# Kernel tuning notes

Hardware: AMD Instinct MI355X
Metric: run time of the kernel (lower is better)

## Reference

```python
import jax, jax.numpy as jnp
import numpy as np

LN_EPS = 1e-5  # torch LayerNorm default
MODES = 4


def setup_inputs() -> dict:
    key = jax.random.key(0)
    ks = jax.random.split(key, 5)
    B, S, H = 4, 4096, 1024
    nh, dk = 16, H // 16
    scale = 1.0 / (H * H)
    # frequency mode selection: random shuffle of range(S//2), take 4, sorted (seeded for determinism)
    rng = np.random.default_rng(0)
    index = jnp.asarray(np.sort(rng.permutation(S // 2)[:MODES]).astype(np.int32))
    return {
        "x": jax.random.normal(ks[0], (B, S, H), dtype=jnp.float32),
        "Wq": jax.random.normal(ks[1], (H, H), dtype=jnp.float32) * np.sqrt(2.0 / (H + dk)),
        "bq": jnp.zeros((H,), dtype=jnp.float32),
        "wr": scale * jax.random.uniform(ks[2], (nh, dk, dk, MODES), dtype=jnp.float32),
        "wi": scale * jax.random.uniform(ks[3], (nh, dk, dk, MODES), dtype=jnp.float32),
        "gamma": jnp.ones((H,), dtype=jnp.float32),
        "beta": jnp.zeros((H,), dtype=jnp.float32),
        "index": index,
    }


def reference(x, Wq, bq, wr, wi, gamma, beta, index):
    B, S, H = x.shape
    nh, dk = wr.shape[0], wr.shape[1]
    # q projection and head split: (B,S,H) -> (B,S,nh,dk) -> (B,nh,dk,S)
    q = (x @ Wq.T + bq).reshape(B, S, nh, dk).transpose(0, 2, 3, 1)
    x_ft = jnp.fft.rfft(q, axis=-1)                 # (B,nh,dk,S//2+1) complex
    xm = x_ft[..., index]                           # gather selected modes: (B,nh,dk,M)
    w = wr + 1j * wi                                # (nh,dk,dk,M) complex
    ym = jnp.einsum('bhim,hiom->bhom', xm, w)       # per-mode complex matmul
    # faithful: results written at slots 0..M-1 of out_ft (loop writes out_ft[...,wi])
    out_ft = jnp.zeros((B, nh, dk, S // 2 + 1), dtype=ym.dtype).at[..., :ym.shape[-1]].set(ym)
    x_if = jnp.fft.irfft(out_ft, n=S, axis=-1)      # (B,nh,dk,S) real
    # faithful permute(0,3,2,1).view: flattens as dk-major over heads
    out = x_if.transpose(0, 3, 2, 1).reshape(B, S, H)
    # dropout is identity in eval mode
    y = out + x
    mu = jnp.mean(y, axis=-1, keepdims=True)
    var = jnp.var(y, axis=-1, keepdims=True)
    return (y - mu) * jax.lax.rsqrt(var + LN_EPS) * gamma + beta
```

## Files before the change

### kernel.cpp

```cpp
#include <hip/hip_runtime.h>
#include <math.h>

#define BB 4
#define SS 4096
#define HH 1024
#define NH 16
#define DK 64
#define NMODES 4
#define NSB 32
#define SCHUNK (SS/NSB)
#define NJB (HH/256)
#define TWO_PI 6.28318530717958647692f

__global__ __launch_bounds__(256) void kA_dft(const float* __restrict__ x,
                                              const int* __restrict__ index,
                                              float* __restrict__ P) {
    __shared__ float tab[SCHUNK * 8];
    int t = threadIdx.x;
    int bid = blockIdx.x;
    int sb = bid & (NSB - 1);
    int jb = (bid >> 5) & (NJB - 1);
    int b  = bid >> 7;

    int kk0 = index[0], kk1 = index[1], kk2 = index[2], kk3 = index[3];
    for (int u = t; u < SCHUNK * NMODES; u += 256) {
        int sl = u >> 2, m = u & 3;
        int k = (m == 0) ? kk0 : (m == 1) ? kk1 : (m == 2) ? kk2 : kk3;
        int sv = sb * SCHUNK + sl;
        int r = (k * sv) & (SS - 1);
        float ang = (float)r * (TWO_PI / (float)SS);
        float sn, cs;
        sincosf(ang, &sn, &cs);
        tab[sl * 8 + m * 2]     = cs;
        tab[sl * 8 + m * 2 + 1] = sn;
    }
    __syncthreads();

    int j = jb * 256 + t;
    float acc[8] = {0.f,0.f,0.f,0.f,0.f,0.f,0.f,0.f};
    const float* xp = x + ((size_t)(b * SS + sb * SCHUNK)) * HH + j;
    for (int r = 0; r < SCHUNK; ++r) {
        float xv = xp[(size_t)r * HH];
        float4 t0 = *(const float4*)&tab[r * 8];
        float4 t1 = *(const float4*)&tab[r * 8 + 4];
        acc[0] += xv * t0.x;  acc[1] -= xv * t0.y;
        acc[2] += xv * t0.z;  acc[3] -= xv * t0.w;
        acc[4] += xv * t1.x;  acc[5] -= xv * t1.y;
        acc[6] += xv * t1.z;  acc[7] -= xv * t1.w;
    }
    float* pp = P + ((size_t)((b * NSB + sb) * HH + j)) * 8;
    *(float4*)pp       = make_float4(acc[0], acc[1], acc[2], acc[3]);
    *(float4*)(pp + 4) = make_float4(acc[4], acc[5], acc[6], acc[7]);
}

__global__ __launch_bounds__(256) void kA2_reduce(const float* __restrict__ P,
                                                  float* __restrict__ G) {
    int g = blockIdx.x * 256 + threadIdx.x;
    int q = g & 7;
    int j = (g >> 3) & (HH - 1);
    int b = g >> 13;
    float s = 0.f;
    for (int sb = 0; sb < NSB; ++sb)
        s += P[((size_t)((b * NSB + sb) * HH + j)) * 8 + q];
    G[g] = s;
}

__global__ __launch_bounds__(256) void kB_proj(const float* __restrict__ Wq,
                                               const float* __restrict__ bq,
                                               const int* __restrict__ index,
                                               const float* __restrict__ G,
                                               float* __restrict__ XM) {
    __shared__ float Gs[HH * 8];
    int t = threadIdx.x;
    int cb = blockIdx.x & 15;
    int b  = blockIdx.x >> 4;
    for (int u = t; u < HH * 8; u += 256) Gs[u] = G[(size_t)b * HH * 8 + u];
    __syncthreads();

    int cl = t >> 2, jq = t & 3;
    int c = cb * 64 + cl;
    float acc[8] = {0.f,0.f,0.f,0.f,0.f,0.f,0.f,0.f};
    for (int j0 = jq * 4; j0 < HH; j0 += 16) {
        float4 wv = *(const float4*)&Wq[(size_t)c * HH + j0];
        const float* gp = &Gs[j0 * 8];
        #pragma unroll
        for (int q = 0; q < 8; ++q) acc[q] += wv.x * gp[q];
        #pragma unroll
        for (int q = 0; q < 8; ++q) acc[q] += wv.y * gp[8 + q];
        #pragma unroll
        for (int q = 0; q < 8; ++q) acc[q] += wv.z * gp[16 + q];
        #pragma unroll
        for (int q = 0; q < 8; ++q) acc[q] += wv.w * gp[24 + q];
    }
    #pragma unroll
    for (int q = 0; q < 8; ++q) {
        acc[q] += __shfl_xor(acc[q], 1);
        acc[q] += __shfl_xor(acc[q], 2);
    }
    if (jq == 0) {
        float bias = bq[c];
        #pragma unroll
        for (int m = 0; m < NMODES; ++m)
            if (index[m] == 0) acc[2 * m] += bias * (float)SS;
        float* o = XM + ((size_t)(b * HH + c)) * 8;
        *(float4*)o       = make_float4(acc[0], acc[1], acc[2], acc[3]);
        *(float4*)(o + 4) = make_float4(acc[4], acc[5], acc[6], acc[7]);
    }
}

#define KC_IQ 8
#define KC_II (DK / KC_IQ)
__global__ __launch_bounds__(512) void kC_modes(const float* __restrict__ wr,
                                                const float* __restrict__ wi,
                                                const float* __restrict__ XM,
                                                float* __restrict__ CF) {
    __shared__ float xs[DK * 8];
    __shared__ float red[KC_IQ][DK][9];
    int t = threadIdx.x;
    int o = t & 63, iq = t >> 6;
    int h = blockIdx.x & 15;
    int b = blockIdx.x >> 4;
    for (int u = t; u < DK * 8; u += 512)
        xs[u] = XM[((size_t)(b * HH + h * DK)) * 8 + u];
    __syncthreads();

    float re[4] = {0.f,0.f,0.f,0.f}, im[4] = {0.f,0.f,0.f,0.f};
    #pragma unroll
    for (int ii = 0; ii < KC_II; ++ii) {
        int i = iq * KC_II + ii;
        float4 wrv = *(const float4*)&wr[(((size_t)(h * DK + i)) * DK + o) * 4];
        float4 wiv = *(const float4*)&wi[(((size_t)(h * DK + i)) * DK + o) * 4];
        float xr, xi;
        xr = xs[i * 8 + 0]; xi = xs[i * 8 + 1];
        re[0] += xr * wrv.x - xi * wiv.x;  im[0] += xr * wiv.x + xi * wrv.x;
        xr = xs[i * 8 + 2]; xi = xs[i * 8 + 3];
        re[1] += xr * wrv.y - xi * wiv.y;  im[1] += xr * wiv.y + xi * wrv.y;
        xr = xs[i * 8 + 4]; xi = xs[i * 8 + 5];
        re[2] += xr * wrv.z - xi * wiv.z;  im[2] += xr * wiv.z + xi * wrv.z;
        xr = xs[i * 8 + 6]; xi = xs[i * 8 + 7];
        re[3] += xr * wrv.w - xi * wiv.w;  im[3] += xr * wiv.w + xi * wrv.w;
    }
    #pragma unroll
    for (int m = 0; m < 4; ++m) {
        red[iq][o][2 * m]     = re[m];
        red[iq][o][2 * m + 1] = im[m];
    }
    __syncthreads();
    if (iq == 0) {
        float rr[8];
        #pragma unroll
        for (int q = 0; q < 8; ++q) {
            float s = 0.f;
            #pragma unroll
            for (int g = 0; g < KC_IQ; ++g) s += red[g][o][q];
            rr[q] = s;
        }
        int co = o * NH + h;
        const float inv = 1.0f / (float)SS;
        float* cp = CF + ((size_t)(b * HH + co)) * 8;
        cp[0] =  rr[0] * inv;
        cp[1] =  2.0f * rr[2] * inv;
        cp[2] = -2.0f * rr[3] * inv;
        cp[3] =  2.0f * rr[4] * inv;
        cp[4] = -2.0f * rr[5] * inv;
        cp[5] =  2.0f * rr[6] * inv;
        cp[6] = -2.0f * rr[7] * inv;
        cp[7] =  0.0f;
    }
}

__global__ __launch_bounds__(256) void kD_out(const float* __restrict__ x,
                                              const float* __restrict__ CF,
                                              const float* __restrict__ gamma,
                                              const float* __restrict__ beta,
                                              float* __restrict__ out) {
    __shared__ float redS[4], redQ[4];
    int t  = threadIdx.x;
    int b  = blockIdx.x >> 8;
    int s0 = (blockIdx.x & 255) * 16;
    int c0 = t * 4;

    const float* cp = CF + (size_t)b * HH * 8 + (size_t)c0 * 8;
    float4 cfa[8];
    #pragma unroll
    for (int e = 0; e < 4; ++e) {
        cfa[2 * e]     = *(const float4*)(cp + e * 8);
        cfa[2 * e + 1] = *(const float4*)(cp + e * 8 + 4);
    }
    float4 g4 = *(const float4*)&gamma[c0];
    float4 b4 = *(const float4*)&beta[c0];

    for (int r = 0; r < 16; ++r) {
        int s = s0 + r;
        float ang = (float)s * (TWO_PI / (float)SS);
        float s1, c1;
        sincosf(ang, &s1, &c1);
        float c2 = c1 * c1 - s1 * s1, s2 = 2.f * s1 * c1;
        float c3 = c2 * c1 - s2 * s1, s3 = s2 * c1 + c2 * s1;

        float4 xv = *(const float4*)&x[((size_t)(b * SS + s)) * HH + c0];
        float y[4];
        #pragma unroll
        for (int e = 0; e < 4; ++e) {
            float xe = (e == 0) ? xv.x : (e == 1) ? xv.y : (e == 2) ? xv.z : xv.w;
            float4 A = cfa[2 * e], Bv = cfa[2 * e + 1];
            y[e] = xe + A.x + A.y * c1 + A.z * s1 + A.w * c2
                      + Bv.x * s2 + Bv.y * c3 + Bv.z * s3;
        }
        float sm = y[0] + y[1] + y[2] + y[3];
        float sq = y[0]*y[0] + y[1]*y[1] + y[2]*y[2] + y[3]*y[3];
        #pragma unroll
        for (int off = 1; off < 64; off <<= 1) {
            sm += __shfl_xor(sm, off);
            sq += __shfl_xor(sq, off);
        }
        int w = t >> 6, lane = t & 63;
        if (lane == 0) { redS[w] = sm; redQ[w] = sq; }
        __syncthreads();
        float tot  = redS[0] + redS[1] + redS[2] + redS[3];
        float totq = redQ[0] + redQ[1] + redQ[2] + redQ[3];
        float mean = tot * (1.0f / (float)HH);
        float var  = totq * (1.0f / (float)HH) - mean * mean;
        float rs = rsqrtf(var + 1e-5f);
        float4 o4;
        o4.x = (y[0] - mean) * rs * g4.x + b4.x;
        o4.y = (y[1] - mean) * rs * g4.y + b4.y;
        o4.z = (y[2] - mean) * rs * g4.z + b4.z;
        o4.w = (y[3] - mean) * rs * g4.w + b4.w;
        *(float4*)&out[((size_t)(b * SS + s)) * HH + c0] = o4;
        __syncthreads();
    }
}

extern "C" void kernel_launch(void* const* d_in, const int* in_sizes, int n_in,
                              void* d_out, int out_size, void* d_ws, size_t ws_size,
                              hipStream_t stream) {
    const float* x     = (const float*)d_in[0];
    const float* Wq    = (const float*)d_in[1];
    const float* bq    = (const float*)d_in[2];
    const float* wr    = (const float*)d_in[3];
    const float* wi    = (const float*)d_in[4];
    const float* gamma = (const float*)d_in[5];
    const float* beta  = (const float*)d_in[6];
    const int*   index = (const int*)d_in[7];
    float* out = (float*)d_out;
    float* ws  = (float*)d_ws;

    const size_t nP     = (size_t)BB * NSB * HH * 8;
    const size_t nSmall = (size_t)BB * HH * 8;

    float *P, *G, *XM, *CF;
    if (ws_size >= (nP + 3 * nSmall) * sizeof(float)) {
        P  = ws;
        G  = P + nP;
        XM = G + nSmall;
        CF = XM + nSmall;
    } else {
        P  = out;
        G  = ws;
        XM = G + nSmall;
        CF = XM + nSmall;
    }

    hipLaunchKernelGGL(kA_dft,     dim3(BB * NJB * NSB), dim3(256), 0, stream, x, index, P);
    hipLaunchKernelGGL(kA2_reduce, dim3(BB * HH * 8 / 256), dim3(256), 0, stream, P, G);
    hipLaunchKernelGGL(kB_proj,    dim3(BB * 16), dim3(256), 0, stream, Wq, bq, index, G, XM);
    hipLaunchKernelGGL(kC_modes,   dim3(BB * NH), dim3(64), 0, stream, wr, wi, XM, CF);
    hipLaunchKernelGGL(kD_out,     dim3(BB * (SS / 16)), dim3(256), 0, stream, x, CF, gamma, beta, out);
}
```

Measured before the change: 71.98 us.

## Vectorize DFT partials with planar layout and batch LayerNorm row reductions

The partial-DFT kernel now has each thread load float4s covering four columns, doubles the number of sequence chunks, and stores partials in a per-coefficient planar layout. The reduce kernel is re-indexed to match. The output LayerNorm kernel now processes 8 rows per reduction round, which cuts the number of block barriers and interleaves shuffle reductions. The mode kernel is launched with 512 threads instead of 64. Together these aim to cut barrier and memory-latency overhead in the two bandwidth-heavy passes over x, at the cost of higher register pressure.

```diff
diff --git a/kernel.cpp b/kernel.cpp
--- a/kernel.cpp
+++ b/kernel.cpp
@@ -7,27 +7,24 @@
 #define NH 16
 #define DK 64
 #define NMODES 4
-#define NSB 32
+#define NSB 64
 #define SCHUNK (SS/NSB)
-#define NJB (HH/256)
+#define PPLANE ((size_t)BB * NSB * HH)
 #define TWO_PI 6.28318530717958647692f
 
 __global__ __launch_bounds__(256) void kA_dft(const float* __restrict__ x,
                                               const int* __restrict__ index,
                                               float* __restrict__ P) {
     __shared__ float tab[SCHUNK * 8];
-    int t = threadIdx.x;
-    int bid = blockIdx.x;
-    int sb = bid & (NSB - 1);
-    int jb = (bid >> 5) & (NJB - 1);
-    int b  = bid >> 7;
-
-    int kk0 = index[0], kk1 = index[1], kk2 = index[2], kk3 = index[3];
-    for (int u = t; u < SCHUNK * NMODES; u += 256) {
-        int sl = u >> 2, m = u & 3;
-        int k = (m == 0) ? kk0 : (m == 1) ? kk1 : (m == 2) ? kk2 : kk3;
+    int t  = threadIdx.x;
+    int sb = blockIdx.x & (NSB - 1);
+    int b  = blockIdx.x >> 6;
+
+    {
+        int sl = t >> 2, m = t & 3;
+        int k  = index[m];
         int sv = sb * SCHUNK + sl;
-        int r = (k * sv) & (SS - 1);
+        int r  = (k * sv) & (SS - 1);
         float ang = (float)r * (TWO_PI / (float)SS);
         float sn, cs;
         sincosf(ang, &sn, &cs);
@@ -36,33 +33,47 @@
     }
     __syncthreads();
 
-    int j = jb * 256 + t;
-    float acc[8] = {0.f,0.f,0.f,0.f,0.f,0.f,0.f,0.f};
-    const float* xp = x + ((size_t)(b * SS + sb * SCHUNK)) * HH + j;
+    int c0 = t * 4;
+    float acc[4][8];
+    #pragma unroll
+    for (int e = 0; e < 4; ++e)
+        #pragma unroll
+        for (int q = 0; q < 8; ++q) acc[e][q] = 0.f;
+
+    const float* xp = x + ((size_t)(b * SS + sb * SCHUNK)) * HH + c0;
+    #pragma unroll 4
     for (int r = 0; r < SCHUNK; ++r) {
-        float xv = xp[(size_t)r * HH];
+        float4 xv = *(const float4*)(xp + (size_t)r * HH);
         float4 t0 = *(const float4*)&tab[r * 8];
         float4 t1 = *(const float4*)&tab[r * 8 + 4];
-        acc[0] += xv * t0.x;  acc[1] -= xv * t0.y;
-        acc[2] += xv * t0.z;  acc[3] -= xv * t0.w;
-        acc[4] += xv * t1.x;  acc[5] -= xv * t1.y;
-        acc[6] += xv * t1.z;  acc[7] -= xv * t1.w;
-    }
-    float* pp = P + ((size_t)((b * NSB + sb) * HH + j)) * 8;
-    *(float4*)pp       = make_float4(acc[0], acc[1], acc[2], acc[3]);
-    *(float4*)(pp + 4) = make_float4(acc[4], acc[5], acc[6], acc[7]);
+        float xe;
+        #pragma unroll
+        for (int e = 0; e < 4; ++e) {
+            xe = (e == 0) ? xv.x : (e == 1) ? xv.y : (e == 2) ? xv.z : xv.w;
+            acc[e][0] += xe * t0.x;  acc[e][1] -= xe * t0.y;
+            acc[e][2] += xe * t0.z;  acc[e][3] -= xe * t0.w;
+            acc[e][4] += xe * t1.x;  acc[e][5] -= xe * t1.y;
+            acc[e][6] += xe * t1.z;  acc[e][7] -= xe * t1.w;
+        }
+    }
+    size_t base = (size_t)(b * NSB + sb) * HH + c0;
+    #pragma unroll
+    for (int q = 0; q < 8; ++q) {
+        *(float4*)&P[q * PPLANE + base] =
+            make_float4(acc[0][q], acc[1][q], acc[2][q], acc[3][q]);
+    }
 }
 
 __global__ __launch_bounds__(256) void kA2_reduce(const float* __restrict__ P,
                                                   float* __restrict__ G) {
     int g = blockIdx.x * 256 + threadIdx.x;
-    int q = g & 7;
-    int j = (g >> 3) & (HH - 1);
+    int j = g & (HH - 1);
+    int q = (g >> 10) & 7;
     int b = g >> 13;
     float s = 0.f;
     for (int sb = 0; sb < NSB; ++sb)
-        s += P[((size_t)((b * NSB + sb) * HH + j)) * 8 + q];
-    G[g] = s;
+        s += P[q * PPLANE + (size_t)(b * NSB + sb) * HH + j];
+    G[((size_t)(b * HH + j)) * 8 + q] = s;
 }
 
 __global__ __launch_bounds__(256) void kB_proj(const float* __restrict__ Wq,
@@ -169,15 +180,17 @@
     }
 }
 
+#define KD_ROWS 16
+#define KD_RB 8
 __global__ __launch_bounds__(256) void kD_out(const float* __restrict__ x,
                                               const float* __restrict__ CF,
                                               const float* __restrict__ gamma,
                                               const float* __restrict__ beta,
                                               float* __restrict__ out) {
-    __shared__ float redS[4], redQ[4];
+    __shared__ float red[4][KD_RB][2];
     int t  = threadIdx.x;
     int b  = blockIdx.x >> 8;
-    int s0 = (blockIdx.x & 255) * 16;
+    int s0 = (blockIdx.x & 255) * KD_ROWS;
     int c0 = t * 4;
 
     const float* cp = CF + (size_t)b * HH * 8 + (size_t)c0 * 8;
@@ -189,45 +202,62 @@
     }
     float4 g4 = *(const float4*)&gamma[c0];
     float4 b4 = *(const float4*)&beta[c0];
-
-    for (int r = 0; r < 16; ++r) {
-        int s = s0 + r;
-        float ang = (float)s * (TWO_PI / (float)SS);
-        float s1, c1;
-        sincosf(ang, &s1, &c1);
-        float c2 = c1 * c1 - s1 * s1, s2 = 2.f * s1 * c1;
-        float c3 = c2 * c1 - s2 * s1, s3 = s2 * c1 + c2 * s1;
-
-        float4 xv = *(const float4*)&x[((size_t)(b * SS + s)) * HH + c0];
-        float y[4];
-        #pragma unroll
-        for (int e = 0; e < 4; ++e) {
-            float xe = (e == 0) ? xv.x : (e == 1) ? xv.y : (e == 2) ? xv.z : xv.w;
-            float4 A = cfa[2 * e], Bv = cfa[2 * e + 1];
-            y[e] = xe + A.x + A.y * c1 + A.z * s1 + A.w * c2
-                      + Bv.x * s2 + Bv.y * c3 + Bv.z * s3;
-        }
-        float sm = y[0] + y[1] + y[2] + y[3];
-        float sq = y[0]*y[0] + y[1]*y[1] + y[2]*y[2] + y[3]*y[3];
+    int w = t >> 6, lane = t & 63;
+
+    for (int batch = 0; batch < KD_ROWS / KD_RB; ++batch) {
+        float y[KD_RB][4], sm[KD_RB], sq[KD_RB];
+        #pragma unroll
+        for (int r = 0; r < KD_RB; ++r) {
+            int s = s0 + batch * KD_RB + r;
+            float ang = (float)s * (TWO_PI / (float)SS);
+            float s1, c1;
+            sincosf(ang, &s1, &c1);
+            float c2 = c1 * c1 - s1 * s1, s2 = 2.f * s1 * c1;
+            float c3 = c2 * c1 - s2 * s1, s3 = s2 * c1 + c2 * s1;
+
+            float4 xv = *(const float4*)&x[((size_t)(b * SS + s)) * HH + c0];
+            #pragma unroll
+            for (int e = 0; e < 4; ++e) {
+                float xe = (e == 0) ? xv.x : (e == 1) ? xv.y : (e == 2) ? xv.z : xv.w;
+                float4 A = cfa[2 * e], Bv = cfa[2 * e + 1];
+                y[r][e] = xe + A.x + A.y * c1 + A.z * s1 + A.w * c2
+                             + Bv.x * s2 + Bv.y * c3 + Bv.z * s3;
+            }
+            sm[r] = y[r][0] + y[r][1] + y[r][2] + y[r][3];
+            sq[r] = y[r][0]*y[r][0] + y[r][1]*y[r][1]
+                  + y[r][2]*y[r][2] + y[r][3]*y[r][3];
+        }
         #pragma unroll
         for (int off = 1; off < 64; off <<= 1) {
-            sm += __shfl_xor(sm, off);
-            sq += __shfl_xor(sq, off);
-        }
-        int w = t >> 6, lane = t & 63;
-        if (lane == 0) { redS[w] = sm; redQ[w] = sq; }
+            #pragma unroll
+            for (int r = 0; r < KD_RB; ++r) {
+                sm[r] += __shfl_xor(sm[r], off);
+                sq[r] += __shfl_xor(sq[r], off);
+            }
+        }
+        if (lane == 0) {
+            #pragma unroll
+            for (int r = 0; r < KD_RB; ++r) {
+                red[w][r][0] = sm[r];
+                red[w][r][1] = sq[r];
+            }
+        }
         __syncthreads();
-        float tot  = redS[0] + redS[1] + redS[2] + redS[3];
-        float totq = redQ[0] + redQ[1] + redQ[2] + redQ[3];
-        float mean = tot * (1.0f / (float)HH);
-        float var  = totq * (1.0f / (float)HH) - mean * mean;
-        float rs = rsqrtf(var + 1e-5f);
-        float4 o4;
-        o4.x = (y[0] - mean) * rs * g4.x + b4.x;
-        o4.y = (y[1] - mean) * rs * g4.y + b4.y;
-        o4.z = (y[2] - mean) * rs * g4.z + b4.z;
-        o4.w = (y[3] - mean) * rs * g4.w + b4.w;
-        *(float4*)&out[((size_t)(b * SS + s)) * HH + c0] = o4;
+        #pragma unroll
+        for (int r = 0; r < KD_RB; ++r) {
+            int s = s0 + batch * KD_RB + r;
+            float tot  = red[0][r][0] + red[1][r][0] + red[2][r][0] + red[3][r][0];
+            float totq = red[0][r][1] + red[1][r][1] + red[2][r][1] + red[3][r][1];
+            float mean = tot * (1.0f / (float)HH);
+            float var  = totq * (1.0f / (float)HH) - mean * mean;
+            float rs = rsqrtf(var + 1e-5f);
+            float4 o4;
+            o4.x = (y[r][0] - mean) * rs * g4.x + b4.x;
+            o4.y = (y[r][1] - mean) * rs * g4.y + b4.y;
+            o4.z = (y[r][2] - mean) * rs * g4.z + b4.z;
+            o4.w = (y[r][3] - mean) * rs * g4.w + b4.w;
+            *(float4*)&out[((size_t)(b * SS + s)) * HH + c0] = o4;
+        }
         __syncthreads();
     }
 }
@@ -246,7 +276,7 @@
     float* out = (float*)d_out;
     float* ws  = (float*)d_ws;
 
-    const size_t nP     = (size_t)BB * NSB * HH * 8;
+    const size_t nP     = PPLANE * 8;
     const size_t nSmall = (size_t)BB * HH * 8;
 
     float *P, *G, *XM, *CF;
@@ -262,9 +292,9 @@
         CF = XM + nSmall;
     }
 
-    hipLaunchKernelGGL(kA_dft,     dim3(BB * NJB * NSB), dim3(256), 0, stream, x, index, P);
+    hipLaunchKernelGGL(kA_dft,     dim3(BB * NSB), dim3(256), 0, stream, x, index, P);
     hipLaunchKernelGGL(kA2_reduce, dim3(BB * HH * 8 / 256), dim3(256), 0, stream, P, G);
     hipLaunchKernelGGL(kB_proj,    dim3(BB * 16), dim3(256), 0, stream, Wq, bq, index, G, XM);
-    hipLaunchKernelGGL(kC_modes,   dim3(BB * NH), dim3(64), 0, stream, wr, wi, XM, CF);
-    hipLaunchKernelGGL(kD_out,     dim3(BB * (SS / 16)), dim3(256), 0, stream, x, CF, gamma, beta, out);
-}
+    hipLaunchKernelGGL(kC_modes,   dim3(BB * NH), dim3(512), 0, stream, wr, wi, XM, CF);
+    hipLaunchKernelGGL(kD_out,     dim3(BB * (SS / KD_ROWS)), dim3(256), 0, stream, x, CF, gamma, beta, out);
+}
```

New measurement: 68.32 us. 1.05x faster.
